# Performance work log

Measured on AMD Instinct MI355X. Metric: run time of the kernel, lower is better.

## Reference

```python
import jax, jax.numpy as jnp
import numpy as np

B, S, D = 8, 1024, 1024

def setup_inputs() -> dict:
    key = jax.random.key(0)
    ks = jax.random.split(key, 6)
    context = jax.random.normal(ks[0], (B, S, D), dtype=jnp.float32)
    eos_mask = jax.random.randint(ks[1], (B, S), 0, 2, dtype=jnp.int32)
    prior = jax.random.uniform(ks[2], (), dtype=jnp.float32)
    adj_mat = jax.random.randint(ks[3], (B, S, S), 0, 2, dtype=jnp.int32)
    Wk = jax.random.normal(ks[4], (D, D), dtype=jnp.float32) * 0.02
    Wq = jax.random.normal(ks[5], (D, D), dtype=jnp.float32) * 0.02
    bk = jnp.zeros((D,), jnp.float32)
    bq = jnp.zeros((D,), jnp.float32)
    ln_gamma = jnp.ones((D,), jnp.float32)
    ln_beta = jnp.zeros((D,), jnp.float32)
    return {"context": context, "eos_mask": eos_mask, "prior": prior,
            "adj_mat": adj_mat, "Wk": Wk, "bk": bk, "Wq": Wq, "bq": bq,
            "ln_gamma": ln_gamma, "ln_beta": ln_beta}

def reference(context, eos_mask, prior, adj_mat, Wk, bk, Wq, bq, ln_gamma, ln_beta):
    d_model = context.shape[-1]
    seq_len = context.shape[1]
    # LayerNorm (annotated-transformer style: unbiased std, eps added to std)
    mu = jnp.mean(context, axis=-1, keepdims=True)
    std = jnp.std(context, axis=-1, keepdims=True, ddof=1)
    x = ln_gamma * (context - mu) / (std + 1e-6) + ln_beta
    # projections (torch Linear: x @ W.T + b)
    key_p = x @ Wk.T + bk
    query = x @ Wq.T + bq
    scores = jnp.einsum('bqd,bkd->bqk', query, key_p) / (d_model / 2)
    scores = jnp.where(adj_mat == 0, -1e9, scores)
    neibor_attn = jax.nn.softmax(scores, axis=-1)
    neibor_attn = jnp.sqrt(neibor_attn * jnp.swapaxes(neibor_attn, -1, -2) + 1e-9)
    neibor_attn = prior + (1.0 - prior) * neibor_attn
    # constant structural matrices
    a = jnp.eye(seq_len, k=1, dtype=jnp.float32)          # superdiagonal
    b = jnp.eye(seq_len, dtype=jnp.float32)               # diagonal
    tri = jnp.triu(jnp.ones((seq_len, seq_len), jnp.float32))  # upper incl diag
    # t = (log(attn+eps) masked to superdiagonal) @ tri
    t = jnp.matmul(jnp.where(a == 0, 0.0, jnp.log(neibor_attn + 1e-9)), tri)
    g_attn = jnp.exp(jnp.matmul(tri, t))
    g_attn = jnp.where((tri - b) == 0, 0.0, g_attn)  # keep strict upper only
    g_attn = g_attn + jnp.swapaxes(g_attn, -1, -2) + jnp.where(b == 0, 1e-9, neibor_attn)
    return (g_attn, neibor_attn)
```

## Files before the change

### kernel.cpp

```cpp
#include <hip/hip_runtime.h>
#include <hip/hip_bf16.h>

#define S_LEN 1024
#define D_DIM 1024
#define N_BAT 8
#define BSS   (8ull*1024ull*1024ull)

using bf16x8 = __attribute__((ext_vector_type(8))) short;
using f32x4  = __attribute__((ext_vector_type(4))) float;

__device__ __forceinline__ short f2bf(float v) {
    __hip_bfloat16 h = __float2bfloat16(v);
    return *reinterpret_cast<short*>(&h);
}

__device__ __forceinline__ void gload_lds16(const void* g, void* l) {
    __builtin_amdgcn_global_load_lds(
        (const __attribute__((address_space(1))) void*)g,
        (__attribute__((address_space(3))) void*)l, 16, 0, 0);
}

__device__ __forceinline__ int xcd_remap_flat() {
    const int nwg  = gridDim.x * gridDim.y * gridDim.z;
    const int flat = blockIdx.x + gridDim.x * (blockIdx.y + gridDim.y * blockIdx.z);
    const int cpx  = nwg >> 3;
    return (flat & 7) * cpx + (flat >> 3);
}

template<int KITERS>
__device__ __forceinline__ void gemm_mainloop_pipe(
    const short* __restrict__ A, const short* __restrict__ Bt,
    int brow, int bcol, int kstart,
    short* As, short* Bs, f32x4 acc[4][2])
{
    const int tid  = threadIdx.x;
    const int lane = tid & 63;
    const int w    = tid >> 6;
    const int wr   = w >> 2;
    const int wc   = w & 3;
    const int rsel = lane & 15;
    const int kb   = (lane >> 4) * 16;

    const int b0   = w * 1024;
    const int b1   = 8192 + w * 1024;
    const int ch0  = b0 + lane * 16;
    const int ch1  = b1 + lane * 16;
    const int row0 = ch0 >> 7;
    const int cb0  = (ch0 & 127) ^ ((row0 & 7) << 4);
    const int row1 = ch1 >> 7;
    const int cb1  = (ch1 & 127) ^ ((row1 & 7) << 4);

#pragma unroll
    for (int m = 0; m < 4; ++m)
#pragma unroll
        for (int n = 0; n < 2; ++n) acc[m][n] = 0.0f;

    constexpr int NPRE = (KITERS < 3) ? KITERS : 3;
#pragma unroll
    for (int i = 0; i < NPRE; ++i) {
        const int k0 = kstart + i * 64;
        char* Ad = (char*)As + i * 16384;
        char* Bd = (char*)Bs + i * 16384;
        gload_lds16((const char*)(A  + (size_t)(brow + row0) * 1024 + k0) + cb0, Ad + b0);
        gload_lds16((const char*)(A  + (size_t)(brow + row1) * 1024 + k0) + cb1, Ad + b1);
        gload_lds16((const char*)(Bt + (size_t)(bcol + row0) * 1024 + k0) + cb0, Bd + b0);
        gload_lds16((const char*)(Bt + (size_t)(bcol + row1) * 1024 + k0) + cb1, Bd + b1);
    }

#pragma unroll
    for (int t = 0; t < KITERS; ++t) {
        const int ahead = KITERS - 1 - t;
        if (ahead >= 2)      asm volatile("s_waitcnt vmcnt(8)" ::: "memory");
        else if (ahead == 1) asm volatile("s_waitcnt vmcnt(4)" ::: "memory");
        else                 asm volatile("s_waitcnt vmcnt(0)" ::: "memory");
        __builtin_amdgcn_s_barrier();
        asm volatile("" ::: "memory");

        if (t + 3 < KITERS) {
            const int k0 = kstart + (t + 3) * 64;
            char* An = (char*)As + ((t + 3) & 3) * 16384;
            char* Bn = (char*)Bs + ((t + 3) & 3) * 16384;
            gload_lds16((const char*)(A  + (size_t)(brow + row0) * 1024 + k0) + cb0, An + b0);
            gload_lds16((const char*)(A  + (size_t)(brow + row1) * 1024 + k0) + cb1, An + b1);
            gload_lds16((const char*)(Bt + (size_t)(bcol + row0) * 1024 + k0) + cb0, Bn + b0);
            gload_lds16((const char*)(Bt + (size_t)(bcol + row1) * 1024 + k0) + cb1, Bn + b1);
        }

        const char* Ac = (const char*)As + (t & 3) * 16384;
        const char* Bc = (const char*)Bs + (t & 3) * 16384;
        bf16x8 af[4][2], bfr[2][2];
#pragma unroll
        for (int m = 0; m < 4; ++m) {
            const int row = wr * 64 + m * 16 + rsel;
            const int sw  = (row & 7) << 4;
#pragma unroll
            for (int kk = 0; kk < 2; ++kk)
                af[m][kk] = *(const bf16x8*)&Ac[row * 128 + ((kk * 64 + kb) ^ sw)];
        }
#pragma unroll
        for (int n = 0; n < 2; ++n) {
            const int row = wc * 32 + n * 16 + rsel;
            const int sw  = (row & 7) << 4;
#pragma unroll
            for (int kk = 0; kk < 2; ++kk)
                bfr[n][kk] = *(const bf16x8*)&Bc[row * 128 + ((kk * 64 + kb) ^ sw)];
        }
#pragma unroll
        for (int kk = 0; kk < 2; ++kk)
#pragma unroll
            for (int m = 0; m < 4; ++m)
#pragma unroll
                for (int n = 0; n < 2; ++n)
                    acc[m][n] = __builtin_amdgcn_mfma_f32_16x16x32_bf16(
                        af[m][kk], bfr[n][kk], acc[m][n], 0, 0, 0);
    }
}

__global__ __launch_bounds__(512) void gemm_bf16(
    const short* __restrict__ A, const short* __restrict__ Bt,
    short* __restrict__ C)
{
    __shared__ short As[4 * 8192];
    __shared__ short Bs[4 * 8192];
    const int nid = xcd_remap_flat();
    const int mx  = ((nid >> 6) << 3) + (nid & 7);
    const int ny  = (nid >> 3) & 7;
    const int brow = mx * 128, bcol = ny * 128;

    f32x4 acc[4][2];
    gemm_mainloop_pipe<16>(A, Bt, brow, bcol, 0, As, Bs, acc);

    const int lane = threadIdx.x & 63;
    const int w    = threadIdx.x >> 6;
    const int wr   = w >> 2, wc = w & 3;
#pragma unroll
    for (int m = 0; m < 4; ++m)
#pragma unroll
        for (int n = 0; n < 2; ++n) {
            const int colg = bcol + wc * 32 + n * 16 + (lane & 15);
#pragma unroll
            for (int r = 0; r < 4; ++r) {
                const int rowg = brow + wr * 64 + m * 16 + ((lane >> 4) * 4 + r);
                C[(size_t)rowg * 1024 + colg] = f2bf(acc[m][n][r]);
            }
        }
}

__global__ __launch_bounds__(512) void gemm_scores(
    const short* __restrict__ Tm, const short* __restrict__ Xm,
    const float* __restrict__ p, const float* __restrict__ r2,
    const float* __restrict__ c0p, float* __restrict__ Sc)
{
    __shared__ short As[4 * 8192];
    __shared__ short Bs[4 * 8192];
    const int nid = xcd_remap_flat();
    const int mx  = nid & 7;
    const int ny  = (nid >> 3) & 7;
    const int b   = nid >> 6;
    const short* A  = Tm + (size_t)b * 1024 * 1024;
    const short* Bt = Xm + (size_t)b * 1024 * 1024;
    const float* pb = p  + (size_t)b * 1024;
    const float* rb = r2 + (size_t)b * 1024;
    float* C = Sc + (size_t)b * 1024 * 1024;
    const int brow = mx * 128, bcol = ny * 128;

    f32x4 acc[4][2];
    gemm_mainloop_pipe<16>(A, Bt, brow, bcol, 0, As, Bs, acc);

    const int lane = threadIdx.x & 63;
    const int w    = threadIdx.x >> 6;
    const int wr   = w >> 2, wc = w & 3;
    const float c0v = c0p[0];
#pragma unroll
    for (int m = 0; m < 4; ++m)
#pragma unroll
        for (int n = 0; n < 2; ++n) {
            const int colg = bcol + wc * 32 + n * 16 + (lane & 15);
            const float radd = rb[colg] + c0v;
#pragma unroll
            for (int r = 0; r < 4; ++r) {
                const int rowg = brow + wr * 64 + m * 16 + ((lane >> 4) * 4 + r);
                C[(size_t)rowg * 1024 + colg] =
                    (acc[m][n][r] + pb[rowg] + radd) * 0.001953125f;
            }
        }
}

__global__ __launch_bounds__(512) void gemm_splitk(
    const short* __restrict__ A, const short* __restrict__ Bt,
    float* __restrict__ P)
{
    __shared__ short As[4 * 8192];
    __shared__ short Bs[4 * 8192];
    const int brow = blockIdx.x * 128, bcol = blockIdx.y * 128;
    const int z = blockIdx.z;

    f32x4 acc[4][2];
    gemm_mainloop_pipe<4>(A, Bt, brow, bcol, z * 256, As, Bs, acc);

    float* Pz = P + (size_t)z * 1024 * 1024;
    const int lane = threadIdx.x & 63;
    const int w    = threadIdx.x >> 6;
    const int wr   = w >> 2, wc = w & 3;
#pragma unroll
    for (int m = 0; m < 4; ++m)
#pragma unroll
        for (int n = 0; n < 2; ++n) {
            const int colg = bcol + wc * 32 + n * 16 + (lane & 15);
#pragma unroll
            for (int r = 0; r < 4; ++r) {
                const int rowg = brow + wr * 64 + m * 16 + ((lane >> 4) * 4 + r);
                Pz[(size_t)rowg * 1024 + colg] = acc[m][n][r];
            }
        }
}

__global__ __launch_bounds__(256) void reduce_m2t(
    const float* __restrict__ P, short* __restrict__ M)
{
    const int idx = blockIdx.x * 256 + threadIdx.x;
    const float4* P4 = (const float4*)P;
    float4 s = P4[idx];
    const float4 s1 = P4[idx + 262144];
    const float4 s2 = P4[idx + 524288];
    const float4 s3 = P4[idx + 786432];
    s.x += s1.x + s2.x + s3.x;
    s.y += s1.y + s2.y + s3.y;
    s.z += s1.z + s2.z + s3.z;
    s.w += s1.w + s2.w + s3.w;
    short4 o;
    o.x = f2bf(s.x); o.y = f2bf(s.y); o.z = f2bf(s.z); o.w = f2bf(s.w);
    ((short4*)M)[idx] = o;
}

__global__ __launch_bounds__(256) void bias_gemv1(
    const float* __restrict__ Wq, const float* __restrict__ Wk,
    const float* __restrict__ bk, const float* __restrict__ bq,
    float* __restrict__ pu, float* __restrict__ pv)
{
    __shared__ float su[8][128];
    __shared__ float sv[8][128];
    const int tx = threadIdx.x & 31;
    const int ty = threadIdx.x >> 5;
    const int colBase = blockIdx.x * 128;
    const int rowBase = blockIdx.y * 64;
    const int i = colBase + tx * 4;
    float4 au = {0,0,0,0}, av = {0,0,0,0};
#pragma unroll
    for (int jj = 0; jj < 8; ++jj) {
        const int j = rowBase + ty + jj * 8;
        const float bkv = bk[j], bqv = bq[j];
        const float4 wq = *(const float4*)&Wq[(size_t)j * 1024 + i];
        const float4 wk = *(const float4*)&Wk[(size_t)j * 1024 + i];
        au.x += wq.x * bkv; au.y += wq.y * bkv; au.z += wq.z * bkv; au.w += wq.w * bkv;
        av.x += wk.x * bqv; av.y += wk.y * bqv; av.z += wk.z * bqv; av.w += wk.w * bqv;
    }
    ((float4*)su[ty])[tx] = au;
    ((float4*)sv[ty])[tx] = av;
    __syncthreads();
    if (ty == 0) {
        float4 s1 = ((float4*)su[0])[tx];
        float4 s2 = ((float4*)sv[0])[tx];
#pragma unroll
        for (int k = 1; k < 8; ++k) {
            const float4 t1 = ((float4*)su[k])[tx];
            const float4 t2 = ((float4*)sv[k])[tx];
            s1.x += t1.x; s1.y += t1.y; s1.z += t1.z; s1.w += t1.w;
            s2.x += t2.x; s2.y += t2.y; s2.z += t2.z; s2.w += t2.w;
        }
        ((float4*)&pu[(size_t)blockIdx.y * 1024 + colBase])[tx] = s1;
        ((float4*)&pv[(size_t)blockIdx.y * 1024 + colBase])[tx] = s2;
    }
}

__global__ __launch_bounds__(256) void bias_gemv2(
    const float* __restrict__ pu, const float* __restrict__ pv,
    const float* __restrict__ bk, const float* __restrict__ bq,
    float* __restrict__ u, float* __restrict__ v, float* __restrict__ c0)
{
    __shared__ float sh[4];
    const int i = blockIdx.x * 256 + threadIdx.x;
    float su = 0.0f, sv = 0.0f;
#pragma unroll
    for (int k = 0; k < 16; ++k) {
        su += pu[k * 1024 + i];
        sv += pv[k * 1024 + i];
    }
    u[i] = su;
    v[i] = sv;
    if (blockIdx.x == 0) {
        const int t = threadIdx.x;
        const float4 a = ((const float4*)bq)[t];
        const float4 b = ((const float4*)bk)[t];
        float s = a.x*b.x + a.y*b.y + a.z*b.z + a.w*b.w;
        for (int off = 32; off > 0; off >>= 1) s += __shfl_down(s, off);
        const int lane = t & 63, w = t >> 6;
        if (lane == 0) sh[w] = s;
        __syncthreads();
        if (t == 0) c0[0] = sh[0] + sh[1] + sh[2] + sh[3];
    }
}

__global__ __launch_bounds__(256) void ln_kernel(
    const float* __restrict__ X, const float* __restrict__ gamma,
    const float* __restrict__ beta, const float* __restrict__ u,
    const float* __restrict__ v2, short* __restrict__ Y,
    float* __restrict__ p, float* __restrict__ r2)
{
    __shared__ float sh[16];
    const size_t row = blockIdx.x;
    const int t = threadIdx.x;
    float4 v = ((const float4*)(X + row * 1024))[t];
    float s  = v.x + v.y + v.z + v.w;
    float ss = v.x*v.x + v.y*v.y + v.z*v.z + v.w*v.w;
    for (int off = 32; off > 0; off >>= 1) {
        s  += __shfl_down(s, off);
        ss += __shfl_down(ss, off);
    }
    const int lane = t & 63, w = t >> 6;
    if (lane == 0) { sh[w] = s; sh[4 + w] = ss; }
    __syncthreads();
    if (t == 0) {
        float S  = sh[0] + sh[1] + sh[2] + sh[3];
        float SS = sh[4] + sh[5] + sh[6] + sh[7];
        float mu = S * (1.0f / 1024.0f);
        float var = fmaxf((SS - S * mu) * (1.0f / 1023.0f), 0.0f);
        sh[0] = mu;
        sh[1] = 1.0f / (sqrtf(var) + 1e-6f);
    }
    __syncthreads();
    const float mu = sh[0], inv = sh[1];
    float4 g  = ((const float4*)gamma)[t];
    float4 be = ((const float4*)beta)[t];
    float y0 = g.x * (v.x - mu) * inv + be.x;
    float y1 = g.y * (v.y - mu) * inv + be.y;
    float y2 = g.z * (v.z - mu) * inv + be.z;
    float y3 = g.w * (v.w - mu) * inv + be.w;
    short4 o;
    o.x = f2bf(y0); o.y = f2bf(y1); o.z = f2bf(y2); o.w = f2bf(y3);
    ((short4*)(Y + row * 1024))[t] = o;
    float4 uu = ((const float4*)u)[t];
    float4 vv = ((const float4*)v2)[t];
    float dp = y0*uu.x + y1*uu.y + y2*uu.z + y3*uu.w;
    float dr = y0*vv.x + y1*vv.y + y2*vv.z + y3*vv.w;
    for (int off = 32; off > 0; off >>= 1) {
        dp += __shfl_down(dp, off);
        dr += __shfl_down(dr, off);
    }
    if (lane == 0) { sh[8 + w] = dp; sh[12 + w] = dr; }
    __syncthreads();
    if (t == 0) {
        p[row]  = sh[8] + sh[9] + sh[10] + sh[11];
        r2[row] = sh[12] + sh[13] + sh[14] + sh[15];
    }
}

__global__ __launch_bounds__(256) void cvt_t_kernel(
    const float* __restrict__ Wq, const float* __restrict__ Wk,
    short* __restrict__ wqt, short* __restrict__ wkt)
{
    __shared__ float T[32][33];
    const float* src = blockIdx.z ? Wk : Wq;
    short* dst = blockIdx.z ? wkt : wqt;
    const int bi = blockIdx.x * 32, bj = blockIdx.y * 32;
    const int c = threadIdx.x & 31, r0 = threadIdx.x >> 5;
#pragma unroll
    for (int rr = 0; rr < 4; ++rr) {
        const int r = r0 + rr * 8;
        T[r][c] = src[(size_t)(bi + r) * 1024 + bj + c];
    }
    __syncthreads();
#pragma unroll
    for (int rr = 0; rr < 4; ++rr) {
        const int r = r0 + rr * 8;
        dst[(size_t)(bj + r) * 1024 + bi + c] = f2bf(T[c][r]);
    }
}

__global__ __launch_bounds__(256) void softmax_kernel(
    const float* __restrict__ Sc, const int* __restrict__ adj,
    float* __restrict__ At)
{
    __shared__ float sh[4];
    const size_t row = blockIdx.x;
    const int t = threadIdx.x;
    const float4 sv = ((const float4*)(Sc + row * 1024))[t];
    const int4   av = ((const int4*)(adj + row * 1024))[t];
    float m = -3.0e38f;
    if (av.x) m = fmaxf(m, sv.x);
    if (av.y) m = fmaxf(m, sv.y);
    if (av.z) m = fmaxf(m, sv.z);
    if (av.w) m = fmaxf(m, sv.w);
    for (int off = 32; off > 0; off >>= 1) m = fmaxf(m, __shfl_down(m, off));
    const int lane = t & 63, w = t >> 6;
    if (lane == 0) sh[w] = m;
    __syncthreads();
    const float M = fmaxf(fmaxf(sh[0], sh[1]), fmaxf(sh[2], sh[3]));
    __syncthreads();
    float e0 = av.x ? expf(sv.x - M) : 0.0f;
    float e1 = av.y ? expf(sv.y - M) : 0.0f;
    float e2 = av.z ? expf(sv.z - M) : 0.0f;
    float e3 = av.w ? expf(sv.w - M) : 0.0f;
    float s = e0 + e1 + e2 + e3;
    for (int off = 32; off > 0; off >>= 1) s += __shfl_down(s, off);
    if (lane == 0) sh[w] = s;
    __syncthreads();
    const float Sm = sh[0] + sh[1] + sh[2] + sh[3];
    float4 o;
    if (Sm > 0.0f) {
        const float inv = 1.0f / Sm;
        o.x = e0 * inv; o.y = e1 * inv; o.z = e2 * inv; o.w = e3 * inv;
    } else {
        o.x = o.y = o.z = o.w = 1.0f / 1024.0f;
    }
    ((float4*)(At + row * 1024))[t] = o;
}

__global__ __launch_bounds__(1024) void cum2_kernel(
    const float* __restrict__ At, const float* __restrict__ prior_p,
    double* __restrict__ cum)
{
    __shared__ double sh[1024];
    const int b = blockIdx.x;
    const int t = threadIdx.x;
    const float prior = *prior_p;
    const float om = 1.0f - prior;
    const float* attn = At + (size_t)b * 1024 * 1024;
    double v = 0.0;
    if (t >= 1) {
        const int k = t - 1;
        const float a1 = attn[(size_t)k * 1024 + (k + 1)];
        const float a2 = attn[(size_t)(k + 1) * 1024 + k];
        const float na = prior + om * sqrtf(a1 * a2 + 1e-9f);
        v = (double)logf(na + 1e-9f);
    }
    sh[t] = v;
    __syncthreads();
#pragma unroll
    for (int off = 1; off < 1024; off <<= 1) {
        const double add = (t >= off) ? sh[t - off] : 0.0;
        __syncthreads();
        sh[t] += add;
        __syncthreads();
    }
    cum[b * 1024 + t] = sh[t];
}

__global__ __launch_bounds__(256) void na_g_kernel(
    float* __restrict__ At, const float* __restrict__ prior_p,
    const double* __restrict__ cum, float* __restrict__ G)
{
    const int ti = blockIdx.x >> 5, tj = blockIdx.x & 31;
    if (tj < ti) return;
    const int b = blockIdx.y;
    const float prior = *prior_p;
    const float om = 1.0f - prior;
    float* base = At + (size_t)b * 1024 * 1024;
    float* gb   = G  + (size_t)b * 1024 * 1024;
    const double* cb = cum + (size_t)b * 1024;
    __shared__ float T1[32][33];
    __shared__ float T2[32][33];
    const int c = threadIdx.x & 31, r0 = threadIdx.x >> 5;
#pragma unroll
    for (int rr = 0; rr < 4; ++rr) {
        const int r = r0 + rr * 8;
        T1[r][c] = base[(size_t)(ti * 32 + r) * 1024 + tj * 32 + c];
        T2[r][c] = base[(size_t)(tj * 32 + r) * 1024 + ti * 32 + c];
    }
    __syncthreads();
#pragma unroll
    for (int rr = 0; rr < 4; ++rr) {
        const int r = r0 + rr * 8;
        const int R1 = ti * 32 + r, C1 = tj * 32 + c;
        const float na1 = prior + om * sqrtf(T1[r][c] * T2[c][r] + 1e-9f);
        base[(size_t)R1 * 1024 + C1] = na1;
        float g1;
        if (R1 == C1) g1 = na1;
        else {
            const int lo = min(R1, C1), hi = max(R1, C1);
            g1 = expf((float)(cb[hi] - cb[lo])) + 1e-9f;
        }
        gb[(size_t)R1 * 1024 + C1] = g1;
        const int R2 = tj * 32 + r, C2 = ti * 32 + c;
        const float na2 = prior + om * sqrtf(T2[r][c] * T1[c][r] + 1e-9f);
        base[(size_t)R2 * 1024 + C2] = na2;
        float g2;
        if (R2 == C2) g2 = na2;
        else {
            const int lo = min(R2, C2), hi = max(R2, C2);
            g2 = expf((float)(cb[hi] - cb[lo])) + 1e-9f;
        }
        gb[(size_t)R2 * 1024 + C2] = g2;
    }
}

extern "C" void kernel_launch(void* const* d_in, const int* in_sizes, int n_in,
                              void* d_out, int out_size, void* d_ws, size_t ws_size,
                              hipStream_t stream)
{
    const float* context = (const float*)d_in[0];
    const float* prior   = (const float*)d_in[2];
    const int*   adj     = (const int*)d_in[3];
    const float* Wk      = (const float*)d_in[4];
    const float* bk      = (const float*)d_in[5];
    const float* Wq      = (const float*)d_in[6];
    const float* bq      = (const float*)d_in[7];
    const float* gamma   = (const float*)d_in[8];
    const float* beta    = (const float*)d_in[9];

    float* out   = (float*)d_out;
    float* gout  = out;
    float* naout = out + BSS;

    char* ws = (char*)d_ws;
    short*  xb    = (short*)(ws);
    short*  wqt   = (short*)(ws + (16ull << 20));
    short*  wkt   = (short*)(ws + (18ull << 20));
    short*  m2t   = (short*)(ws + (20ull << 20));
    short*  tb    = (short*)(ws + (22ull << 20));
    float*  m2par = (float*)tb;
    double* cumd  = (double*)(ws + (38ull << 20));
    float*  uvec  = (float*)(ws + (38ull << 20) + (1ull << 16));
    float*  vvec  = uvec + 1024;
    float*  c0    = vvec + 1024;
    float*  pvec  = c0 + 64;
    float*  rvec  = pvec + 8192;
    float*  pu    = rvec + 8192;
    float*  pv    = pu + 16384;

    bias_gemv1<<<dim3(8, 16), 256, 0, stream>>>(Wq, Wk, bk, bq, pu, pv);
    bias_gemv2<<<4, 256, 0, stream>>>(pu, pv, bk, bq, uvec, vvec, c0);
    ln_kernel<<<8192, 256, 0, stream>>>(context, gamma, beta, uvec, vvec,
                                        xb, pvec, rvec);
    cvt_t_kernel<<<dim3(32, 32, 2), 256, 0, stream>>>(Wq, Wk, wqt, wkt);
    gemm_splitk<<<dim3(8, 8, 4), 512, 0, stream>>>(wkt, wqt, m2par);
    reduce_m2t<<<1024, 256, 0, stream>>>(m2par, m2t);
    gemm_bf16<<<dim3(64, 8), 512, 0, stream>>>(xb, m2t, tb);
    gemm_scores<<<dim3(8, 8, 8), 512, 0, stream>>>(tb, xb, pvec, rvec, c0, gout);
    softmax_kernel<<<8192, 256, 0, stream>>>(gout, adj, naout);
    cum2_kernel<<<8, 1024, 0, stream>>>(naout, prior, cumd);
    na_g_kernel<<<dim3(1024, 8), 256, 0, stream>>>(naout, prior, cumd, gout);
}
```

Measured before the change: 137.9 us.

## Enlarge GEMM tiles to 256x128 with 3-stage LDS pipeline and MFMA priority

Rewrites the shared bf16 GEMM mainloop to compute 256x128 output tiles per 512-thread block, so each of the 8 waves owns a 64x64 sub-tile instead of 64x32. The LDS pipeline drops from 4 stages to 3, and the next stage's loads are issued after the fragment reads, with s_setprio raised around the MFMA block. The larger tiles raise arithmetic intensity and reuse of each global load. In exchange, the grids get half as many blocks (256 for the main GEMMs, 128 for split-K), which may underfill the GPU's CUs, and register pressure rises from the doubled accumulators. The XCD block remapping is also rewritten for the new grid shapes.

```diff
diff --git a/kernel.cpp b/kernel.cpp
--- a/kernel.cpp
+++ b/kernel.cpp
@@ -20,99 +20,87 @@
         (__attribute__((address_space(3))) void*)l, 16, 0, 0);
 }
 
-__device__ __forceinline__ int xcd_remap_flat() {
-    const int nwg  = gridDim.x * gridDim.y * gridDim.z;
-    const int flat = blockIdx.x + gridDim.x * (blockIdx.y + gridDim.y * blockIdx.z);
-    const int cpx  = nwg >> 3;
-    return (flat & 7) * cpx + (flat >> 3);
-}
-
 template<int KITERS>
-__device__ __forceinline__ void gemm_mainloop_pipe(
+__device__ __forceinline__ void gemm_mainloop256(
     const short* __restrict__ A, const short* __restrict__ Bt,
     int brow, int bcol, int kstart,
-    short* As, short* Bs, f32x4 acc[4][2])
+    short* As, short* Bs, f32x4 acc[4][4])
 {
     const int tid  = threadIdx.x;
     const int lane = tid & 63;
     const int w    = tid >> 6;
-    const int wr   = w >> 2;
-    const int wc   = w & 3;
+    const int wr   = w >> 1;
+    const int wc   = w & 1;
     const int rsel = lane & 15;
     const int kb   = (lane >> 4) * 16;
-
-    const int b0   = w * 1024;
-    const int b1   = 8192 + w * 1024;
-    const int ch0  = b0 + lane * 16;
-    const int ch1  = b1 + lane * 16;
-    const int row0 = ch0 >> 7;
-    const int cb0  = (ch0 & 127) ^ ((row0 & 7) << 4);
-    const int row1 = ch1 >> 7;
-    const int cb1  = (ch1 & 127) ^ ((row1 & 7) << 4);
+    const int sw   = (rsel & 7) << 4;
+
+    const int srow  = tid >> 3;
+    const int scolb = ((tid & 7) * 16) ^ ((srow & 7) << 4);
+    const int sdst  = tid * 16;
 
 #pragma unroll
     for (int m = 0; m < 4; ++m)
 #pragma unroll
-        for (int n = 0; n < 2; ++n) acc[m][n] = 0.0f;
-
-    constexpr int NPRE = (KITERS < 3) ? KITERS : 3;
-#pragma unroll
-    for (int i = 0; i < NPRE; ++i) {
-        const int k0 = kstart + i * 64;
-        char* Ad = (char*)As + i * 16384;
-        char* Bd = (char*)Bs + i * 16384;
-        gload_lds16((const char*)(A  + (size_t)(brow + row0) * 1024 + k0) + cb0, Ad + b0);
-        gload_lds16((const char*)(A  + (size_t)(brow + row1) * 1024 + k0) + cb1, Ad + b1);
-        gload_lds16((const char*)(Bt + (size_t)(bcol + row0) * 1024 + k0) + cb0, Bd + b0);
-        gload_lds16((const char*)(Bt + (size_t)(bcol + row1) * 1024 + k0) + cb1, Bd + b1);
-    }
+        for (int n = 0; n < 4; ++n) acc[m][n] = 0.0f;
+
+    auto stage = [&](int slot, int k0) {
+        char* Ad = (char*)As + slot * 32768;
+        char* Bd = (char*)Bs + slot * 16384;
+#pragma unroll
+        for (int c = 0; c < 4; ++c) {
+            const int row = c * 64 + srow;
+            gload_lds16((const char*)(A + (size_t)(brow + row) * 1024 + k0) + scolb,
+                        Ad + c * 8192 + sdst);
+        }
+#pragma unroll
+        for (int c = 0; c < 2; ++c) {
+            const int row = c * 64 + srow;
+            gload_lds16((const char*)(Bt + (size_t)(bcol + row) * 1024 + k0) + scolb,
+                        Bd + c * 8192 + sdst);
+        }
+    };
+
+    stage(0, kstart);
+    if (KITERS > 1) stage(1, kstart + 64);
 
 #pragma unroll
     for (int t = 0; t < KITERS; ++t) {
-        const int ahead = KITERS - 1 - t;
-        if (ahead >= 2)      asm volatile("s_waitcnt vmcnt(8)" ::: "memory");
-        else if (ahead == 1) asm volatile("s_waitcnt vmcnt(4)" ::: "memory");
-        else                 asm volatile("s_waitcnt vmcnt(0)" ::: "memory");
+        if (t < KITERS - 1) asm volatile("s_waitcnt vmcnt(6)" ::: "memory");
+        else                asm volatile("s_waitcnt vmcnt(0)" ::: "memory");
         __builtin_amdgcn_s_barrier();
         asm volatile("" ::: "memory");
 
-        if (t + 3 < KITERS) {
-            const int k0 = kstart + (t + 3) * 64;
-            char* An = (char*)As + ((t + 3) & 3) * 16384;
-            char* Bn = (char*)Bs + ((t + 3) & 3) * 16384;
-            gload_lds16((const char*)(A  + (size_t)(brow + row0) * 1024 + k0) + cb0, An + b0);
-            gload_lds16((const char*)(A  + (size_t)(brow + row1) * 1024 + k0) + cb1, An + b1);
-            gload_lds16((const char*)(Bt + (size_t)(bcol + row0) * 1024 + k0) + cb0, Bn + b0);
-            gload_lds16((const char*)(Bt + (size_t)(bcol + row1) * 1024 + k0) + cb1, Bn + b1);
-        }
-
-        const char* Ac = (const char*)As + (t & 3) * 16384;
-        const char* Bc = (const char*)Bs + (t & 3) * 16384;
-        bf16x8 af[4][2], bfr[2][2];
+        const char* Ac = (const char*)As + (t % 3) * 32768;
+        const char* Bc = (const char*)Bs + (t % 3) * 16384;
+        bf16x8 af[4][2], bfr[4][2];
 #pragma unroll
         for (int m = 0; m < 4; ++m) {
             const int row = wr * 64 + m * 16 + rsel;
-            const int sw  = (row & 7) << 4;
 #pragma unroll
             for (int kk = 0; kk < 2; ++kk)
                 af[m][kk] = *(const bf16x8*)&Ac[row * 128 + ((kk * 64 + kb) ^ sw)];
         }
 #pragma unroll
-        for (int n = 0; n < 2; ++n) {
-            const int row = wc * 32 + n * 16 + rsel;
-            const int sw  = (row & 7) << 4;
+        for (int n = 0; n < 4; ++n) {
+            const int row = wc * 64 + n * 16 + rsel;
 #pragma unroll
             for (int kk = 0; kk < 2; ++kk)
                 bfr[n][kk] = *(const bf16x8*)&Bc[row * 128 + ((kk * 64 + kb) ^ sw)];
         }
+
+        if (t + 2 < KITERS) stage((t + 2) % 3, kstart + (t + 2) * 64);
+
+        __builtin_amdgcn_s_setprio(1);
 #pragma unroll
         for (int kk = 0; kk < 2; ++kk)
 #pragma unroll
             for (int m = 0; m < 4; ++m)
 #pragma unroll
-                for (int n = 0; n < 2; ++n)
+                for (int n = 0; n < 4; ++n)
                     acc[m][n] = __builtin_amdgcn_mfma_f32_16x16x32_bf16(
                         af[m][kk], bfr[n][kk], acc[m][n], 0, 0, 0);
+        __builtin_amdgcn_s_setprio(0);
     }
 }
 
@@ -120,24 +108,25 @@
     const short* __restrict__ A, const short* __restrict__ Bt,
     short* __restrict__ C)
 {
-    __shared__ short As[4 * 8192];
-    __shared__ short Bs[4 * 8192];
-    const int nid = xcd_remap_flat();
-    const int mx  = ((nid >> 6) << 3) + (nid & 7);
-    const int ny  = (nid >> 3) & 7;
-    const int brow = mx * 128, bcol = ny * 128;
-
-    f32x4 acc[4][2];
-    gemm_mainloop_pipe<16>(A, Bt, brow, bcol, 0, As, Bs, acc);
+    __shared__ short As[3 * 16384];
+    __shared__ short Bs[3 * 8192];
+    const int flat = blockIdx.x + 32 * blockIdx.y;
+    const int nid  = (flat & 7) * 32 + (flat >> 3);
+    const int mx   = nid >> 3;
+    const int ny   = nid & 7;
+    const int brow = mx * 256, bcol = ny * 128;
+
+    f32x4 acc[4][4];
+    gemm_mainloop256<16>(A, Bt, brow, bcol, 0, As, Bs, acc);
 
     const int lane = threadIdx.x & 63;
     const int w    = threadIdx.x >> 6;
-    const int wr   = w >> 2, wc = w & 3;
+    const int wr   = w >> 1, wc = w & 1;
 #pragma unroll
     for (int m = 0; m < 4; ++m)
 #pragma unroll
-        for (int n = 0; n < 2; ++n) {
-            const int colg = bcol + wc * 32 + n * 16 + (lane & 15);
+        for (int n = 0; n < 4; ++n) {
+            const int colg = bcol + wc * 64 + n * 16 + (lane & 15);
 #pragma unroll
             for (int r = 0; r < 4; ++r) {
                 const int rowg = brow + wr * 64 + m * 16 + ((lane >> 4) * 4 + r);
@@ -151,31 +140,33 @@
     const float* __restrict__ p, const float* __restrict__ r2,
     const float* __restrict__ c0p, float* __restrict__ Sc)
 {
-    __shared__ short As[4 * 8192];
-    __shared__ short Bs[4 * 8192];
-    const int nid = xcd_remap_flat();
-    const int mx  = nid & 7;
-    const int ny  = (nid >> 3) & 7;
-    const int b   = nid >> 6;
+    __shared__ short As[3 * 16384];
+    __shared__ short Bs[3 * 8192];
+    const int flat = blockIdx.x + 4 * blockIdx.y + 32 * blockIdx.z;
+    const int nid  = (flat & 7) * 32 + (flat >> 3);
+    const int b    = nid >> 5;
+    const int rem  = nid & 31;
+    const int mx   = rem & 3;
+    const int ny   = rem >> 2;
     const short* A  = Tm + (size_t)b * 1024 * 1024;
     const short* Bt = Xm + (size_t)b * 1024 * 1024;
     const float* pb = p  + (size_t)b * 1024;
     const float* rb = r2 + (size_t)b * 1024;
     float* C = Sc + (size_t)b * 1024 * 1024;
-    const int brow = mx * 128, bcol = ny * 128;
-
-    f32x4 acc[4][2];
-    gemm_mainloop_pipe<16>(A, Bt, brow, bcol, 0, As, Bs, acc);
+    const int brow = mx * 256, bcol = ny * 128;
+
+    f32x4 acc[4][4];
+    gemm_mainloop256<16>(A, Bt, brow, bcol, 0, As, Bs, acc);
 
     const int lane = threadIdx.x & 63;
     const int w    = threadIdx.x >> 6;
-    const int wr   = w >> 2, wc = w & 3;
+    const int wr   = w >> 1, wc = w & 1;
     const float c0v = c0p[0];
 #pragma unroll
     for (int m = 0; m < 4; ++m)
 #pragma unroll
-        for (int n = 0; n < 2; ++n) {
-            const int colg = bcol + wc * 32 + n * 16 + (lane & 15);
+        for (int n = 0; n < 4; ++n) {
+            const int colg = bcol + wc * 64 + n * 16 + (lane & 15);
             const float radd = rb[colg] + c0v;
 #pragma unroll
             for (int r = 0; r < 4; ++r) {
@@ -190,23 +181,23 @@
     const short* __restrict__ A, const short* __restrict__ Bt,
     float* __restrict__ P)
 {
-    __shared__ short As[4 * 8192];
-    __shared__ short Bs[4 * 8192];
-    const int brow = blockIdx.x * 128, bcol = blockIdx.y * 128;
+    __shared__ short As[3 * 16384];
+    __shared__ short Bs[3 * 8192];
+    const int brow = blockIdx.x * 256, bcol = blockIdx.y * 128;
     const int z = blockIdx.z;
 
-    f32x4 acc[4][2];
-    gemm_mainloop_pipe<4>(A, Bt, brow, bcol, z * 256, As, Bs, acc);
+    f32x4 acc[4][4];
+    gemm_mainloop256<4>(A, Bt, brow, bcol, z * 256, As, Bs, acc);
 
     float* Pz = P + (size_t)z * 1024 * 1024;
     const int lane = threadIdx.x & 63;
     const int w    = threadIdx.x >> 6;
-    const int wr   = w >> 2, wc = w & 3;
+    const int wr   = w >> 1, wc = w & 1;
 #pragma unroll
     for (int m = 0; m < 4; ++m)
 #pragma unroll
-        for (int n = 0; n < 2; ++n) {
-            const int colg = bcol + wc * 32 + n * 16 + (lane & 15);
+        for (int n = 0; n < 4; ++n) {
+            const int colg = bcol + wc * 64 + n * 16 + (lane & 15);
 #pragma unroll
             for (int r = 0; r < 4; ++r) {
                 const int rowg = brow + wr * 64 + m * 16 + ((lane >> 4) * 4 + r);
@@ -533,10 +524,10 @@
     ln_kernel<<<8192, 256, 0, stream>>>(context, gamma, beta, uvec, vvec,
                                         xb, pvec, rvec);
     cvt_t_kernel<<<dim3(32, 32, 2), 256, 0, stream>>>(Wq, Wk, wqt, wkt);
-    gemm_splitk<<<dim3(8, 8, 4), 512, 0, stream>>>(wkt, wqt, m2par);
+    gemm_splitk<<<dim3(4, 8, 4), 512, 0, stream>>>(wkt, wqt, m2par);
     reduce_m2t<<<1024, 256, 0, stream>>>(m2par, m2t);
-    gemm_bf16<<<dim3(64, 8), 512, 0, stream>>>(xb, m2t, tb);
-    gemm_scores<<<dim3(8, 8, 8), 512, 0, stream>>>(tb, xb, pvec, rvec, c0, gout);
+    gemm_bf16<<<dim3(32, 8), 512, 0, stream>>>(xb, m2t, tb);
+    gemm_scores<<<dim3(4, 8, 8), 512, 0, stream>>>(tb, xb, pvec, rvec, c0, gout);
     softmax_kernel<<<8192, 256, 0, stream>>>(gout, adj, naout);
     cum2_kernel<<<8, 1024, 0, stream>>>(naout, prior, cumd);
     na_g_kernel<<<dim3(1024, 8), 256, 0, stream>>>(naout, prior, cumd, gout);
```

After: 132.6 us. -3.8%, faster.
